# Optimization experiments

Hardware: AMD Instinct MI355X
Metric: run time of the kernel (lower is better)

Reference implementation:

```python
import jax, jax.numpy as jnp
import numpy as np

N = 8192
F_IN = 256
F_OUT = 256


def setup_inputs() -> dict:
    key = jax.random.key(0)
    k1, k2, k3 = jax.random.split(key, 3)
    H = jax.random.normal(k1, (N, F_IN), dtype=jnp.float32)
    A_tilde = jax.random.uniform(k2, (N, N), dtype=jnp.float32)  # positive -> valid degrees
    # xavier_uniform for W: limit = sqrt(6/(fan_in+fan_out))
    limit = np.sqrt(6.0 / (F_IN + F_OUT)).astype(np.float32)
    W = jax.random.uniform(k3, (F_IN, F_OUT), dtype=jnp.float32, minval=-limit, maxval=limit)
    return {"H": H, "A_tilde": A_tilde, "W": W}


def reference(H, A_tilde, W):
    # H(l+1) = relu(D^-1/2 A D^-1/2 H W)
    # Diagonal matmuls expressed as row/col rescaling (same math, O(N^2)).
    d_inv_sqrt = jnp.sum(A_tilde, axis=1) ** -0.5          # [N]
    A_norm = d_inv_sqrt[:, None] * A_tilde * d_inv_sqrt[None, :]  # [N,N]
    H_next = (A_norm @ H) @ W                              # [N,F_out]
    return jax.nn.relu(H_next)
```

## Files before the change

### kernel.cpp

```cpp
#include <hip/hip_runtime.h>
#include <hip/hip_bf16.h>

#define N_ROWS 8192
#define F_DIM  256
#define KSPLIT 4

typedef __bf16 bf16x8_t __attribute__((ext_vector_type(8)));
typedef float  f32x4_t  __attribute__((ext_vector_type(4)));

static __device__ __forceinline__ unsigned short f2bf(float x) {
    union { __hip_bfloat16 h; unsigned short u; } c;
    c.h = __float2bfloat16(x);
    return c.u;
}
static __device__ __forceinline__ unsigned pk2(float lo, float hi) {
    return (unsigned)f2bf(lo) | ((unsigned)f2bf(hi) << 16);
}

static __device__ __forceinline__ void gload16(const unsigned short* g, unsigned short* s) {
    __builtin_amdgcn_global_load_lds((const __attribute__((address_space(1))) void*)g,
                                     (__attribute__((address_space(3))) void*)s, 16, 0, 0);
}

__global__ __launch_bounds__(256) void wconv_kernel(const float* __restrict__ W,
                                                    unsigned short* __restrict__ Ws) {
    const int kb = blockIdx.x;
    const int t  = threadIdx.x;
    __shared__ float wt[32][257];
    const int r = t >> 3, g = t & 7;
    const float* src = W + (kb * 32 + r) * F_DIM + g * 32;
#pragma unroll
    for (int i = 0; i < 8; ++i) {
        float4 v = *(const float4*)(src + i * 4);
        wt[r][g * 32 + i * 4 + 0] = v.x;
        wt[r][g * 32 + i * 4 + 1] = v.y;
        wt[r][g * 32 + i * 4 + 2] = v.z;
        wt[r][g * 32 + i * 4 + 3] = v.w;
    }
    __syncthreads();
    unsigned o[16];
#pragma unroll
    for (int k = 0; k < 32; k += 2) o[k >> 1] = pk2(wt[k][t], wt[k + 1][t]);
    uint4* dst = (uint4*)(Ws + kb * 8192 + t * 32);
#pragma unroll
    for (int i = 0; i < 4; ++i) dst[i] = make_uint4(o[4*i], o[4*i+1], o[4*i+2], o[4*i+3]);
}

__global__ __launch_bounds__(1024) void sumconv_kernel(const float* __restrict__ A,
                                                       const float* __restrict__ H,
                                                       float* __restrict__ dvec,
                                                       unsigned short* __restrict__ Abf,
                                                       unsigned short* __restrict__ Xrm) {
    const int kb = blockIdx.x;
    const int t  = threadIdx.x;
    __shared__ float psum[32][33];
    __shared__ float dl[32];

    const int r = t >> 5, g = t & 31;
    const int row = kb * 32 + r;
    const float* arow = A + (size_t)row * N_ROWS;
    unsigned short* aout = Abf + (size_t)row * N_ROWS;
    float s0 = 0.f, s1 = 0.f, s2 = 0.f, s3 = 0.f;
#pragma unroll 8
    for (int i = 0; i < 64; ++i) {
        const int e = (i * 32 + g) * 4;
        float4 v = *(const float4*)(arow + e);
        s0 += v.x; s1 += v.y; s2 += v.z; s3 += v.w;
        uint2 p = make_uint2(pk2(v.x, v.y), pk2(v.z, v.w));
        *(uint2*)(aout + e) = p;
    }
    psum[r][g] = (s0 + s1) + (s2 + s3);
    __syncthreads();
    if (t < 32) {
        float s = 0.f;
#pragma unroll
        for (int i = 0; i < 32; ++i) s += psum[t][i];
        float d = 1.0f / sqrtf(s);
        dl[t] = d;
        dvec[kb * 32 + t] = d;
    }
    __syncthreads();
    {
        const int hr = t >> 5, hg = t & 31;
        const int hrow = kb * 32 + hr;
        const float* hsrc = H + (size_t)hrow * F_DIM + hg * 8;
        float4 v0 = ((const float4*)hsrc)[0];
        float4 v1 = ((const float4*)hsrc)[1];
        const float d = dl[hr];
        uint4 o = make_uint4(pk2(v0.x * d, v0.y * d), pk2(v0.z * d, v0.w * d),
                             pk2(v1.x * d, v1.y * d), pk2(v1.z * d, v1.w * d));
        *(uint4*)(Xrm + (size_t)hrow * F_DIM + hg * 8) = o;
    }
}

__global__ __launch_bounds__(256) void x2gemm_kernel(const unsigned short* __restrict__ Xrm,
                                                     const unsigned short* __restrict__ Ws,
                                                     unsigned short* __restrict__ X2s) {
    const int t = threadIdx.x;
    const int w = t >> 6, l = t & 63;
    const int m16 = l & 15, q = l >> 4, q8 = q * 8;
    const int rbase = blockIdx.x * 64 + w * 16;

    f32x4_t acc[16] = {};
    const unsigned short* ap = Xrm + (size_t)(rbase + m16) * F_DIM + q8;
#pragma unroll
    for (int kb = 0; kb < 8; ++kb) {
        bf16x8_t af = __builtin_bit_cast(bf16x8_t, *(const uint4*)(ap + kb * 32));
        const unsigned short* bp = Ws + kb * 8192 + m16 * 32 + q8;
#pragma unroll
        for (int nt = 0; nt < 16; ++nt) {
            bf16x8_t bf = __builtin_bit_cast(bf16x8_t, *(const uint4*)(bp + nt * 512));
            acc[nt] = __builtin_amdgcn_mfma_f32_16x16x32_bf16(af, bf, acc[nt], 0, 0, 0);
        }
    }
    const int kr0 = rbase + q * 4;
    unsigned short* op = X2s + (kr0 >> 5) * 8192 + m16 * 32 + (kr0 & 31);
#pragma unroll
    for (int nt = 0; nt < 16; ++nt) {
        uint2 o = make_uint2(pk2(acc[nt][0], acc[nt][1]), pk2(acc[nt][2], acc[nt][3]));
        *(uint2*)(op + nt * 512) = o;
    }
}

__global__ __launch_bounds__(256, 2) void biggemm_kernel(const unsigned short* __restrict__ Abf,
                                                         const unsigned short* __restrict__ X2s,
                                                         float* __restrict__ Ypart) {
    const int t = threadIdx.x;
    const int w = t >> 6, l = t & 63;
    const int m16 = l & 15, q = l >> 4, q8 = q * 8;
    const int bid = blockIdx.x;
    const int ks = bid & 3, mi = bid >> 2;
    const int kbase = ks * 2048;

    __shared__ __align__(16) unsigned short lds[2][4096];

    const unsigned short* ag[2];
    int aslot[2];
#pragma unroll
    for (int j = 0; j < 2; ++j) {
        const int idx = w * 2 + j, ft = idx >> 1, s = idx & 1;
        ag[j] = Abf + (size_t)(mi * 64 + ft * 16 + m16) * N_ROWS + kbase + s * 32 + q8;
        aslot[j] = idx * 512;
    }
    const unsigned short* bptr = X2s + (kbase >> 5) * 8192 + (w * 64 + m16) * 32 + q8;

    f32x4_t acc[4][4] = {};

#pragma unroll
    for (int j = 0; j < 2; ++j) gload16(ag[j], &lds[0][aslot[j]]);
    uint4 bcur[2][4];
#pragma unroll
    for (int s = 0; s < 2; ++s)
#pragma unroll
        for (int nt = 0; nt < 4; ++nt)
            bcur[s][nt] = *(const uint4*)(bptr + s * 8192 + nt * 512);

    const int KITERS = 2048 / 64;
    for (int i = 0; i < KITERS; ++i) {
        __syncthreads();
        const int cb = i & 1;
        uint4 bnxt[2][4];
        if (i + 1 < KITERS) {
#pragma unroll
            for (int j = 0; j < 2; ++j)
                gload16(ag[j] + (i + 1) * 64, &lds[cb ^ 1][aslot[j]]);
            const unsigned short* bp = bptr + (i + 1) * 16384;
#pragma unroll
            for (int s = 0; s < 2; ++s)
#pragma unroll
                for (int nt = 0; nt < 4; ++nt)
                    bnxt[s][nt] = *(const uint4*)(bp + s * 8192 + nt * 512);
        }
#pragma unroll
        for (int s = 0; s < 2; ++s) {
            bf16x8_t af[4];
#pragma unroll
            for (int mt = 0; mt < 4; ++mt)
                af[mt] = *(const bf16x8_t*)&lds[cb][(mt * 2 + s) * 512 + l * 8];
#pragma unroll
            for (int mt = 0; mt < 4; ++mt)
#pragma unroll
                for (int nt = 0; nt < 4; ++nt)
                    acc[mt][nt] = __builtin_amdgcn_mfma_f32_16x16x32_bf16(
                        af[mt], __builtin_bit_cast(bf16x8_t, bcur[s][nt]), acc[mt][nt], 0, 0, 0);
        }
#pragma unroll
        for (int s = 0; s < 2; ++s)
#pragma unroll
            for (int nt = 0; nt < 4; ++nt)
                bcur[s][nt] = bnxt[s][nt];
    }

    float* Y = Ypart + (size_t)ks * (N_ROWS * F_DIM);
#pragma unroll
    for (int mt = 0; mt < 4; ++mt) {
#pragma unroll
        for (int r = 0; r < 4; ++r) {
            const int row = mi * 64 + mt * 16 + q * 4 + r;
#pragma unroll
            for (int nt = 0; nt < 4; ++nt) {
                const int col = w * 64 + nt * 16 + m16;
                Y[(size_t)row * F_DIM + col] = acc[mt][nt][r];
            }
        }
    }
}

__global__ __launch_bounds__(256) void reduce_kernel(const float* __restrict__ Ypart,
                                                     const float* __restrict__ dvec,
                                                     float* __restrict__ out) {
    const int idx = blockIdx.x * 256 + threadIdx.x;
    const int row = idx >> 6;
    const float d = dvec[row];
    const size_t YS = (size_t)N_ROWS * F_DIM / 4;
    const float4* yp = (const float4*)Ypart;
    float4 a = yp[idx];
    float4 b = yp[idx + YS];
    float4 c = yp[idx + 2 * YS];
    float4 e = yp[idx + 3 * YS];
    float4 o;
    o.x = fmaxf(d * (a.x + b.x + c.x + e.x), 0.f);
    o.y = fmaxf(d * (a.y + b.y + c.y + e.y), 0.f);
    o.z = fmaxf(d * (a.z + b.z + c.z + e.z), 0.f);
    o.w = fmaxf(d * (a.w + b.w + c.w + e.w), 0.f);
    ((float4*)out)[idx] = o;
}

extern "C" void kernel_launch(void* const* d_in, const int* in_sizes, int n_in,
                              void* d_out, int out_size, void* d_ws, size_t ws_size,
                              hipStream_t stream) {
    (void)in_sizes; (void)n_in; (void)out_size; (void)ws_size;
    const float* H = (const float*)d_in[0];
    const float* A = (const float*)d_in[1];
    const float* W = (const float*)d_in[2];
    float* out = (float*)d_out;

    char* ws = (char*)d_ws;
    size_t off = 0;
    float*          dvec = (float*)(ws + off);           off += (32 << 10);
    unsigned short* Xrm  = (unsigned short*)(ws + off);  off += (4 << 20);
    unsigned short* Wsz  = (unsigned short*)(ws + off);  off += (128 << 10);
    unsigned short* X2s  = (unsigned short*)(ws + off);  off += (4 << 20);
    float*          Yp   = (float*)(ws + off);           off += (size_t)KSPLIT * N_ROWS * F_DIM * 4;
    unsigned short* Abf  = (unsigned short*)(ws + off);  off += (size_t)N_ROWS * N_ROWS * 2;

    wconv_kernel  <<<dim3(8),    dim3(256),  0, stream>>>(W, Wsz);
    sumconv_kernel<<<dim3(256),  dim3(1024), 0, stream>>>(A, H, dvec, Abf, Xrm);
    x2gemm_kernel <<<dim3(128),  dim3(256),  0, stream>>>(Xrm, Wsz, X2s);
    biggemm_kernel<<<dim3(512),  dim3(256),  0, stream>>>(Abf, X2s, Yp);
    reduce_kernel <<<dim3(2048), dim3(256),  0, stream>>>(Yp, dvec, out);
}
```

Before: 522.3 us.

## Load big GEMM fragments directly to registers and fuse H scaling into x2gemm

The big GEMM no longer stages A tiles through shared memory with per-iteration barriers. Each wave now loads its A and B fragments directly from global memory into registers, double-buffered across k-steps. Separately, the H row scaling and bf16 conversion move into the X·W GEMM, removing an intermediate buffer and its write and read. The trade-off is that each wave now re-reads the same A rows that other waves in the block also read, instead of sharing them via LDS, which raises global/L2 traffic in exchange for fewer syncs.

New measurement: 516.8 us. Within noise of the previous version (-1.1%).

```diff
diff --git a/kernel.cpp b/kernel.cpp
--- a/kernel.cpp
+++ b/kernel.cpp
@@ -15,11 +15,6 @@
 }
 static __device__ __forceinline__ unsigned pk2(float lo, float hi) {
     return (unsigned)f2bf(lo) | ((unsigned)f2bf(hi) << 16);
-}
-
-static __device__ __forceinline__ void gload16(const unsigned short* g, unsigned short* s) {
-    __builtin_amdgcn_global_load_lds((const __attribute__((address_space(1))) void*)g,
-                                     (__attribute__((address_space(3))) void*)s, 16, 0, 0);
 }
 
 __global__ __launch_bounds__(256) void wconv_kernel(const float* __restrict__ W,
@@ -47,14 +42,11 @@
 }
 
 __global__ __launch_bounds__(1024) void sumconv_kernel(const float* __restrict__ A,
-                                                       const float* __restrict__ H,
                                                        float* __restrict__ dvec,
-                                                       unsigned short* __restrict__ Abf,
-                                                       unsigned short* __restrict__ Xrm) {
+                                                       unsigned short* __restrict__ Abf) {
     const int kb = blockIdx.x;
     const int t  = threadIdx.x;
     __shared__ float psum[32][33];
-    __shared__ float dl[32];
 
     const int r = t >> 5, g = t & 31;
     const int row = kb * 32 + r;
@@ -75,25 +67,12 @@
         float s = 0.f;
 #pragma unroll
         for (int i = 0; i < 32; ++i) s += psum[t][i];
-        float d = 1.0f / sqrtf(s);
-        dl[t] = d;
-        dvec[kb * 32 + t] = d;
-    }
-    __syncthreads();
-    {
-        const int hr = t >> 5, hg = t & 31;
-        const int hrow = kb * 32 + hr;
-        const float* hsrc = H + (size_t)hrow * F_DIM + hg * 8;
-        float4 v0 = ((const float4*)hsrc)[0];
-        float4 v1 = ((const float4*)hsrc)[1];
-        const float d = dl[hr];
-        uint4 o = make_uint4(pk2(v0.x * d, v0.y * d), pk2(v0.z * d, v0.w * d),
-                             pk2(v1.x * d, v1.y * d), pk2(v1.z * d, v1.w * d));
-        *(uint4*)(Xrm + (size_t)hrow * F_DIM + hg * 8) = o;
-    }
-}
-
-__global__ __launch_bounds__(256) void x2gemm_kernel(const unsigned short* __restrict__ Xrm,
+        dvec[kb * 32 + t] = 1.0f / sqrtf(s);
+    }
+}
+
+__global__ __launch_bounds__(256) void x2gemm_kernel(const float* __restrict__ H,
+                                                     const float* __restrict__ dvec,
                                                      const unsigned short* __restrict__ Ws,
                                                      unsigned short* __restrict__ X2s) {
     const int t = threadIdx.x;
@@ -102,10 +81,16 @@
     const int rbase = blockIdx.x * 64 + w * 16;
 
     f32x4_t acc[16] = {};
-    const unsigned short* ap = Xrm + (size_t)(rbase + m16) * F_DIM + q8;
+    const int arow = rbase + m16;
+    const float d = dvec[arow];
+    const float* ap = H + (size_t)arow * F_DIM + q8;
 #pragma unroll
     for (int kb = 0; kb < 8; ++kb) {
-        bf16x8_t af = __builtin_bit_cast(bf16x8_t, *(const uint4*)(ap + kb * 32));
+        float4 u0 = *(const float4*)(ap + kb * 32);
+        float4 u1 = *(const float4*)(ap + kb * 32 + 4);
+        uint4 aw = make_uint4(pk2(u0.x * d, u0.y * d), pk2(u0.z * d, u0.w * d),
+                              pk2(u1.x * d, u1.y * d), pk2(u1.z * d, u1.w * d));
+        bf16x8_t af = __builtin_bit_cast(bf16x8_t, aw);
         const unsigned short* bp = Ws + kb * 8192 + m16 * 32 + q8;
 #pragma unroll
         for (int nt = 0; nt < 16; ++nt) {
@@ -120,6 +105,29 @@
         uint2 o = make_uint2(pk2(acc[nt][0], acc[nt][1]), pk2(acc[nt][2], acc[nt][3]));
         *(uint2*)(op + nt * 512) = o;
     }
+}
+
+struct Frag { uint4 a[4]; uint4 b[4]; };
+
+static __device__ __forceinline__ void load_step(Frag& f,
+                                                 const unsigned short* aB,
+                                                 const unsigned short* bB, int s) {
+#pragma unroll
+    for (int mt = 0; mt < 4; ++mt)
+        f.a[mt] = *(const uint4*)(aB + (size_t)mt * 16 * N_ROWS + s * 32);
+#pragma unroll
+    for (int nt = 0; nt < 4; ++nt)
+        f.b[nt] = *(const uint4*)(bB + nt * 512 + (size_t)s * 8192);
+}
+
+static __device__ __forceinline__ void compute_step(f32x4_t acc[4][4], const Frag& f) {
+#pragma unroll
+    for (int mt = 0; mt < 4; ++mt)
+#pragma unroll
+        for (int nt = 0; nt < 4; ++nt)
+            acc[mt][nt] = __builtin_amdgcn_mfma_f32_16x16x32_bf16(
+                __builtin_bit_cast(bf16x8_t, f.a[mt]),
+                __builtin_bit_cast(bf16x8_t, f.b[nt]), acc[mt][nt], 0, 0, 0);
 }
 
 __global__ __launch_bounds__(256, 2) void biggemm_kernel(const unsigned short* __restrict__ Abf,
@@ -132,63 +140,21 @@
     const int ks = bid & 3, mi = bid >> 2;
     const int kbase = ks * 2048;
 
-    __shared__ __align__(16) unsigned short lds[2][4096];
-
-    const unsigned short* ag[2];
-    int aslot[2];
-#pragma unroll
-    for (int j = 0; j < 2; ++j) {
-        const int idx = w * 2 + j, ft = idx >> 1, s = idx & 1;
-        ag[j] = Abf + (size_t)(mi * 64 + ft * 16 + m16) * N_ROWS + kbase + s * 32 + q8;
-        aslot[j] = idx * 512;
-    }
-    const unsigned short* bptr = X2s + (kbase >> 5) * 8192 + (w * 64 + m16) * 32 + q8;
+    const unsigned short* aB = Abf + (size_t)(mi * 64 + m16) * N_ROWS + kbase + q8;
+    const unsigned short* bB = X2s + (kbase >> 5) * 8192 + (w * 64 + m16) * 32 + q8;
 
     f32x4_t acc[4][4] = {};
 
-#pragma unroll
-    for (int j = 0; j < 2; ++j) gload16(ag[j], &lds[0][aslot[j]]);
-    uint4 bcur[2][4];
-#pragma unroll
-    for (int s = 0; s < 2; ++s)
-#pragma unroll
-        for (int nt = 0; nt < 4; ++nt)
-            bcur[s][nt] = *(const uint4*)(bptr + s * 8192 + nt * 512);
-
-    const int KITERS = 2048 / 64;
-    for (int i = 0; i < KITERS; ++i) {
-        __syncthreads();
-        const int cb = i & 1;
-        uint4 bnxt[2][4];
-        if (i + 1 < KITERS) {
-#pragma unroll
-            for (int j = 0; j < 2; ++j)
-                gload16(ag[j] + (i + 1) * 64, &lds[cb ^ 1][aslot[j]]);
-            const unsigned short* bp = bptr + (i + 1) * 16384;
-#pragma unroll
-            for (int s = 0; s < 2; ++s)
-#pragma unroll
-                for (int nt = 0; nt < 4; ++nt)
-                    bnxt[s][nt] = *(const uint4*)(bp + s * 8192 + nt * 512);
-        }
-#pragma unroll
-        for (int s = 0; s < 2; ++s) {
-            bf16x8_t af[4];
-#pragma unroll
-            for (int mt = 0; mt < 4; ++mt)
-                af[mt] = *(const bf16x8_t*)&lds[cb][(mt * 2 + s) * 512 + l * 8];
-#pragma unroll
-            for (int mt = 0; mt < 4; ++mt)
-#pragma unroll
-                for (int nt = 0; nt < 4; ++nt)
-                    acc[mt][nt] = __builtin_amdgcn_mfma_f32_16x16x32_bf16(
-                        af[mt], __builtin_bit_cast(bf16x8_t, bcur[s][nt]), acc[mt][nt], 0, 0, 0);
-        }
-#pragma unroll
-        for (int s = 0; s < 2; ++s)
-#pragma unroll
-            for (int nt = 0; nt < 4; ++nt)
-                bcur[s][nt] = bnxt[s][nt];
+    Frag f0, f1;
+    load_step(f0, aB, bB, 0);
+    load_step(f1, aB, bB, 1);
+
+    const int STEPS = 2048 / 32;
+    for (int s = 0; s < STEPS; s += 2) {
+        compute_step(acc, f0);
+        if (s + 2 < STEPS) load_step(f0, aB, bB, s + 2);
+        compute_step(acc, f1);
+        if (s + 3 < STEPS) load_step(f1, aB, bB, s + 3);
     }
 
     float* Y = Ypart + (size_t)ks * (N_ROWS * F_DIM);
@@ -238,15 +204,14 @@
     char* ws = (char*)d_ws;
     size_t off = 0;
     float*          dvec = (float*)(ws + off);           off += (32 << 10);
-    unsigned short* Xrm  = (unsigned short*)(ws + off);  off += (4 << 20);
     unsigned short* Wsz  = (unsigned short*)(ws + off);  off += (128 << 10);
     unsigned short* X2s  = (unsigned short*)(ws + off);  off += (4 << 20);
     float*          Yp   = (float*)(ws + off);           off += (size_t)KSPLIT * N_ROWS * F_DIM * 4;
     unsigned short* Abf  = (unsigned short*)(ws + off);  off += (size_t)N_ROWS * N_ROWS * 2;
 
     wconv_kernel  <<<dim3(8),    dim3(256),  0, stream>>>(W, Wsz);
-    sumconv_kernel<<<dim3(256),  dim3(1024), 0, stream>>>(A, H, dvec, Abf, Xrm);
-    x2gemm_kernel <<<dim3(128),  dim3(256),  0, stream>>>(Xrm, Wsz, X2s);
+    sumconv_kernel<<<dim3(256),  dim3(1024), 0, stream>>>(A, dvec, Abf);
+    x2gemm_kernel <<<dim3(128),  dim3(256),  0, stream>>>(H, dvec, Wsz, X2s);
     biggemm_kernel<<<dim3(512),  dim3(256),  0, stream>>>(Abf, X2s, Yp);
     reduce_kernel <<<dim3(2048), dim3(256),  0, stream>>>(Yp, dvec, out);
 }
```
